# Kernel optimization log

Measured on AMD Instinct MI355X. Metric: run time of the kernel, lower is better.

Reference implementation:

```python
import jax, jax.numpy as jnp
import numpy as np

V_SIZE, E, H = 30000, 256, 128   # vocab, emb_dim, GRU hidden per direction
B, U, T, ND = 32, 32, 128, 64    # dialogues, utterances, max tokens, dialogue-id table size
SCALE = E ** 0.5                  # attention normalise_factor = hid_size**0.5, hid_size = emb_dim


def _gru_dir(x_seq, w_ih, w_hh, b_ih, b_hh):
    """Unidirectional torch-style GRU. x_seq: [N,T,E] -> [N,T,H]."""
    xp = jnp.einsum('nte,ge->ntg', x_seq, w_ih) + b_ih   # precompute input gates [N,T,3H]
    xp = jnp.swapaxes(xp, 0, 1)                          # [T,N,3H]

    def step(h, xpt):
        gh = h @ w_hh.T + b_hh
        r = jax.nn.sigmoid(xpt[:, :H] + gh[:, :H])
        z = jax.nn.sigmoid(xpt[:, H:2 * H] + gh[:, H:2 * H])
        n = jnp.tanh(xpt[:, 2 * H:] + r * gh[:, 2 * H:])
        h_new = (1.0 - z) * n + z * h
        return h_new, h_new

    h0 = jnp.zeros((x_seq.shape[0], H), x_seq.dtype)
    _, out = jax.lax.scan(step, h0, xp)
    return jnp.swapaxes(out, 0, 1)


def _forward(x, d_ids, utt_len, emb_table,
             w_ih_f, w_hh_f, b_ih_f, b_hh_f,
             w_ih_b, w_hh_b, b_ih_b, b_hh_b,
             wq, bq, wk, bk, wv, bv, wo, bo, wl, bl):
    b, u, t = x.shape
    N = b * u
    emb = emb_table[x.reshape(N, t)]                      # [N,T,E]
    lens = jnp.clip(utt_len[d_ids].reshape(N), 1, t)      # valid tokens per utterance
    pos = jnp.arange(t)
    # index map that reverses the valid prefix (padding region clipped, unused)
    rev_idx = jnp.clip(lens[:, None] - 1 - pos[None, :], 0, t - 1)  # [N,T]

    o_f = _gru_dir(emb, w_ih_f, w_hh_f, b_ih_f, b_hh_f)   # causal => correct on valid prefix
    emb_rev = jnp.take_along_axis(emb, rev_idx[:, :, None], axis=1)
    o_b = jnp.take_along_axis(_gru_dir(emb_rev, w_ih_b, w_hh_b, b_ih_b, b_hh_b),
                              rev_idx[:, :, None], axis=1)
    h = jnp.concatenate([o_f, o_b], axis=-1)              # [N,T,E] bi-GRU states

    # self-attention pooling; original takes op[-1], so only the query at the
    # last valid token (lens-1) is needed -- identical math, less compute.
    k = jnp.einsum('nte,he->nth', h, wk) + bk
    v = jnp.einsum('nte,he->nth', h, wv) + bv
    h_last = jnp.take_along_axis(h, (lens - 1)[:, None, None], axis=1)[:, 0]  # [N,E]
    q = h_last @ wq.T + bq
    score = jnp.einsum('nh,nth->nt', q, k) / SCALE
    score = jnp.where(pos[None, :] < lens[:, None], score, -jnp.inf)
    attn = jax.nn.softmax(score, axis=-1)
    ctx = jnp.einsum('nt,nth->nh', attn, v)
    out = (ctx @ wo.T + bo) @ wl.T + bl                   # make_output then final linear
    return out.reshape(b, u, -1)


def setup_inputs() -> dict:
    key = jax.random.key(0)
    ks = jax.random.split(key, 16)

    def p(k, shape):
        return (jax.random.normal(k, shape, jnp.float32) / np.sqrt(shape[-1])).astype(jnp.float32)

    return {
        'x': jax.random.randint(ks[0], (B, U, T), 0, V_SIZE, dtype=jnp.int32),
        'd_ids': jax.random.randint(ks[1], (B,), 0, ND, dtype=jnp.int32),
        'utt_len': jax.random.randint(ks[2], (ND, U), 1, T + 1, dtype=jnp.int32),
        'emb_table': p(ks[3], (V_SIZE, E)),
        'w_ih_f': p(ks[4], (3 * H, E)), 'w_hh_f': p(ks[5], (3 * H, H)),
        'b_ih_f': jnp.zeros(3 * H, jnp.float32), 'b_hh_f': jnp.zeros(3 * H, jnp.float32),
        'w_ih_b': p(ks[6], (3 * H, E)), 'w_hh_b': p(ks[7], (3 * H, H)),
        'b_ih_b': jnp.zeros(3 * H, jnp.float32), 'b_hh_b': jnp.zeros(3 * H, jnp.float32),
        'wq': p(ks[8], (E, E)), 'bq': jnp.zeros(E, jnp.float32),
        'wk': p(ks[9], (E, E)), 'bk': jnp.zeros(E, jnp.float32),
        'wv': p(ks[10], (E, E)), 'bv': jnp.zeros(E, jnp.float32),
        'wo': p(ks[11], (E, E)), 'bo': jnp.zeros(E, jnp.float32),
        'wl': p(ks[12], (E, E)), 'bl': jnp.zeros(E, jnp.float32),
    }


def reference(x, d_ids, utt_len, emb_table,
              w_ih_f, w_hh_f, b_ih_f, b_hh_f,
              w_ih_b, w_hh_b, b_ih_b, b_hh_b,
              wq, bq, wk, bk, wv, bv, wo, bo, wl, bl):
    return _forward(x, d_ids, utt_len, emb_table,
                    w_ih_f, w_hh_f, b_ih_f, b_hh_f,
                    w_ih_b, w_hh_b, b_ih_b, b_hh_b,
                    wq, bq, wk, bk, wv, bv, wo, bo, wl, bl)
```

## Files before the change

### kernel.cpp

```cpp
#include <hip/hip_runtime.h>
#include <hip/hip_bf16.h>
#include <math.h>
#include <stdint.h>

typedef unsigned short u16;
typedef unsigned int   u32;
typedef __attribute__((ext_vector_type(8))) short bf16x8;
typedef __attribute__((ext_vector_type(4))) float f32x4;

#define EDIM 256
#define HDIM 128
#define TLEN 128
#define NUTT 1024
#define UU   32
#define NBU  8

#define WS_FLAG 0
#define WS_LENS 64
#define WS_TAB  4608
#define WS_COPY 8192
#define WS_OF   18874368LL
#define WS_OB   52428800LL

#define MFMA16(a, b, c) __builtin_amdgcn_mfma_f32_16x16x32_bf16((a), (b), (c), 0, 0, 0)
#define SOUT(u, s, j) ((u) * 1096 + (s) * 136 + (j))

__constant__ int G_SZ[18] = {7680000, 98304, 49152, 384, 384, 98304, 49152, 384, 384,
                             65536, 256, 65536, 65536, 256, 65536, 256, 65536, 256};

__device__ __forceinline__ float b2f(u16 b) {
    u32 u = ((u32)b) << 16; float f; __builtin_memcpy(&f, &u, 4); return f;
}
__device__ __forceinline__ u16 f2b(float f) {
    u32 u; __builtin_memcpy(&u, &f, 4);
    u32 r = u + 0x7FFFu + ((u >> 16) & 1u);
    return (u16)(r >> 16);
}
__device__ __forceinline__ u16 f2b_hw(float f) {
    __hip_bfloat16 h = __float2bfloat16(f);
    u16 v; __builtin_memcpy(&v, &h, 2); return v;
}
__device__ __forceinline__ float fsigmoid(float x) { return 1.0f / (1.0f + __expf(-x)); }
__device__ __forceinline__ float ftanh(float x) { return 1.0f - 2.0f / (__expf(2.0f * x) + 1.0f); }

__global__ __launch_bounds__(256)
void k_convert(void* ws,
               const int* __restrict__ d_ids, const int* __restrict__ utt_len,
               const void* a0, const void* a1, const void* a2, const void* a3,
               const void* a4, const void* a5, const void* a6, const void* a7,
               const void* a8, const void* a9, const void* a10, const void* a11,
               const void* a12, const void* a13, const void* a14, const void* a15,
               const void* a16, const void* a17) {
    __shared__ int scnt[4];
    const int tid = threadIdx.x, lane = tid & 63, wid = tid >> 6;
    const u16* p = (const u16*)a0;
    int cnt = 0;
#pragma unroll 8
    for (int i = tid; i < 16384; i += 256)
        cnt += ((p[i] & 0x7F80) == 0x7F80) ? 1 : 0;
#pragma unroll
    for (int o = 32; o > 0; o >>= 1) cnt += __shfl_down(cnt, o);
    if (lane == 0) scnt[wid] = cnt;
    __syncthreads();
    const int flag = (scnt[0] + scnt[1] + scnt[2] + scnt[3] > 0) ? 1 : 0;

    if (blockIdx.x == 0) {
        if (tid == 0) {
            const void* orig[18] = {a0,a1,a2,a3,a4,a5,a6,a7,a8,a9,a10,a11,a12,a13,a14,a15,a16,a17};
            *(int*)((char*)ws + WS_FLAG) = flag;
            const u16** tab = (const u16**)((char*)ws + WS_TAB);
            char* base = (char*)ws + WS_COPY;
            long long cum = 0;
            for (int a = 0; a < 18; ++a) {
                tab[a] = flag ? (const u16*)(base + cum * 2) : (const u16*)orig[a];
                cum += G_SZ[a];
            }
        }
        int* lens = (int*)((char*)ws + WS_LENS);
#pragma unroll 4
        for (int n = tid; n < NUTT; n += 256) {
            int b = n >> 5;
            int u = n & (UU - 1);
            int L = utt_len[d_ids[b] * UU + u];
            lens[n] = min(max(L, 1), TLEN);
        }
    }

    if (flag == 0) return;
    const void* orig[18] = {a0,a1,a2,a3,a4,a5,a6,a7,a8,a9,a10,a11,a12,a13,a14,a15,a16,a17};
    u16* base = (u16*)((char*)ws + WS_COPY);
    const int gtid = blockIdx.x * blockDim.x + tid;
    const int gs   = gridDim.x * blockDim.x;
    long long cum = 0;
    for (int a = 0; a < 18; ++a) {
        const float4* src = (const float4*)orig[a];
        uint2* dst = (uint2*)(base + cum);
        const int n4 = G_SZ[a] >> 2;
        for (int i = gtid; i < n4; i += gs) {
            float4 v = src[i];
            uint2 pk;
            pk.x = (u32)f2b(v.x) | ((u32)f2b(v.y) << 16);
            pk.y = (u32)f2b(v.z) | ((u32)f2b(v.w) << 16);
            dst[i] = pk;
        }
        cum += G_SZ[a];
    }
}

__global__ __launch_bounds__(512)
void k_scan(const int* __restrict__ x, void* ws) {
    const u16* const* tab = (const u16* const*)((char*)ws + WS_TAB);
    const int dir = blockIdx.y;
    const u16* emb  = tab[0];
    const u16* w_ih = tab[1 + dir * 4];
    const u16* w_hh = tab[2 + dir * 4];
    const u16* b_ih = tab[3 + dir * 4];
    const u16* b_hh = tab[4 + dir * 4];
    u16* outp = (u16*)((char*)ws + (dir ? WS_OB : WS_OF));
    const int* lens = (const int*)((char*)ws + WS_LENS);

    const int n0 = blockIdx.x * NBU;
    __shared__ __align__(16) u16 sh_emb[2][NBU][264];
    __shared__ __align__(16) u16 sh_hi[2][NBU * 136];
    __shared__ __align__(16) u16 sh_lo[2][NBU * 136];
    __shared__ __align__(16) u16 sh_out[2][NBU * 1096];
    __shared__ int sh_tok[NBU * 132];
    __shared__ int sh_L[NBU];

    const int tid = threadIdx.x, lane = tid & 63, wvi = tid >> 6;
    const int q4 = lane >> 4, mm = lane & 15;
    const int j = wvi * 16 + mm;
    const int u8 = mm & 7;

    for (int i = tid; i < NBU * 136; i += 512) { sh_hi[0][i] = 0; sh_lo[0][i] = 0; }
    for (int i = tid; i < NBU * TLEN; i += 512) {
        const int u = i >> 7, tt = i & 127;
        sh_tok[u * 132 + tt] = x[(n0 + u) * TLEN + tt];
    }
    if (tid < NBU) sh_L[tid] = lens[n0 + tid];

    bf16x8 wih[3][8]; bf16x8 whh[3][4];
    float bcr, bcz, bxn, bgn;
#pragma unroll
    for (int n3 = 0; n3 < 3; ++n3) {
        const int g = n3 * HDIM + j;
#pragma unroll
        for (int ks = 0; ks < 8; ++ks)
            wih[n3][ks] = *(const bf16x8*)(w_ih + g * EDIM + ks * 32 + q4 * 8);
#pragma unroll
        for (int ks = 0; ks < 4; ++ks)
            whh[n3][ks] = *(const bf16x8*)(w_hh + g * HDIM + ks * 32 + q4 * 8);
    }
    bcr = b2f(b_ih[j]) + b2f(b_hh[j]);
    bcz = b2f(b_ih[HDIM + j]) + b2f(b_hh[HDIM + j]);
    bxn = b2f(b_ih[2 * HDIM + j]);
    bgn = b2f(b_hh[2 * HDIM + j]);

    const int arr0 = (q4 & 2);
    float hprev[2] = {0.f, 0.f};
    const f32x4 zero4 = {0.f, 0.f, 0.f, 0.f};
    __syncthreads();

    int Lm = sh_L[0];
#pragma unroll
    for (int u = 1; u < NBU; ++u) Lm = max(Lm, sh_L[u]);
    const int tmax = (Lm + 7) & ~7;

    const bool pwave = (wvi < 4);
    const int pf_u = lane & 7;
    const int pf_c = wvi * 8 + (lane >> 3);
    const int pf_L = sh_L[pf_u];

    uint4 pf;
    if (pwave) {
        const int te0 = dir ? (pf_L - 1) : 0;
        const int tok0 = sh_tok[pf_u * 132 + te0];
        uint4 v0 = *(const uint4*)(emb + (size_t)tok0 * EDIM + pf_c * 8);
        *(uint4*)&sh_emb[0][pf_u][pf_c * 8] = v0;
        const int te1 = dir ? max(pf_L - 2, 0) : 1;
        const int tok1 = sh_tok[pf_u * 132 + te1];
        uint4 v1 = *(const uint4*)(emb + (size_t)tok1 * EDIM + pf_c * 8);
        *(uint4*)&sh_emb[1][pf_u][pf_c * 8] = v1;
    }
    __syncthreads();

    f32x4 accx_cur[3];
    {
        bf16x8 a = *(const bf16x8*)&sh_emb[0][u8][q4 * 8];
#pragma unroll
        for (int n3 = 0; n3 < 3; ++n3) accx_cur[n3] = MFMA16(a, wih[n3][0], zero4);
#pragma unroll
        for (int ks = 1; ks < 8; ++ks) {
            bf16x8 a2 = *(const bf16x8*)&sh_emb[0][u8][ks * 32 + q4 * 8];
#pragma unroll
            for (int n3 = 0; n3 < 3; ++n3) accx_cur[n3] = MFMA16(a2, wih[n3][ks], accx_cur[n3]);
        }
    }
    __syncthreads();

    for (int t = 0; t < tmax; ++t) {
        const int cur = t & 1, nxt = cur ^ 1;
        const int obuf = (t >> 3) & 1, slot = t & 7;
        const bool more = (t + 2 < tmax);

        if (pwave && more) {
            const int te = dir ? max(pf_L - 3 - t, 0) : (t + 2);
            const int tok = sh_tok[pf_u * 132 + te];
            pf = *(const uint4*)(emb + (size_t)tok * EDIM + pf_c * 8);
        }

        f32x4 accg[3];
        {
            bf16x8 ahi = *(const bf16x8*)(sh_hi[cur] + u8 * 136 + q4 * 8);
            bf16x8 alo = *(const bf16x8*)(sh_lo[cur] + u8 * 136 + q4 * 8);
#pragma unroll
            for (int n3 = 0; n3 < 3; ++n3) {
                accg[n3] = MFMA16(ahi, whh[n3][0], zero4);
                accg[n3] = MFMA16(alo, whh[n3][0], accg[n3]);
            }
        }
#pragma unroll
        for (int ks = 1; ks < 4; ++ks) {
            bf16x8 ahi = *(const bf16x8*)(sh_hi[cur] + u8 * 136 + ks * 32 + q4 * 8);
            bf16x8 alo = *(const bf16x8*)(sh_lo[cur] + u8 * 136 + ks * 32 + q4 * 8);
#pragma unroll
            for (int n3 = 0; n3 < 3; ++n3) {
                accg[n3] = MFMA16(ahi, whh[n3][ks], accg[n3]);
                accg[n3] = MFMA16(alo, whh[n3][ks], accg[n3]);
            }
        }

        f32x4 accx_nxt[3];
        if (t + 1 < tmax) {
            bf16x8 a = *(const bf16x8*)&sh_emb[nxt][u8][q4 * 8];
#pragma unroll
            for (int n3 = 0; n3 < 3; ++n3) accx_nxt[n3] = MFMA16(a, wih[n3][0], zero4);
#pragma unroll
            for (int ks = 1; ks < 8; ++ks) {
                bf16x8 a2 = *(const bf16x8*)&sh_emb[nxt][u8][ks * 32 + q4 * 8];
#pragma unroll
                for (int n3 = 0; n3 < 3; ++n3) accx_nxt[n3] = MFMA16(a2, wih[n3][ks], accx_nxt[n3]);
            }
        }

#pragma unroll
        for (int rr2 = 0; rr2 < 2; ++rr2) {
            const int arr = rr2 + arr0;
            const int u   = (q4 * 4 + arr) & 7;
            const float r  = fsigmoid(accx_cur[0][arr] + accg[0][arr] + bcr);
            const float z  = fsigmoid(accx_cur[1][arr] + accg[1][arr] + bcz);
            const float nn = ftanh((accx_cur[2][arr] + bxn) + r * (accg[2][arr] + bgn));
            const float hn = (1.0f - z) * nn + z * hprev[rr2];
            hprev[rr2] = hn;
            const u16 hb = f2b_hw(hn);
            sh_hi[nxt][u * 136 + j] = hb;
            sh_lo[nxt][u * 136 + j] = f2b_hw(hn - b2f(hb));
            sh_out[obuf][SOUT(u, slot, j)] = hb;
        }

        if (pwave && more)
            *(uint4*)&sh_emb[cur][pf_u][pf_c * 8] = pf;

        if (t + 1 < tmax) {
#pragma unroll
            for (int n3 = 0; n3 < 3; ++n3) accx_cur[n3] = accx_nxt[n3];
        }

        __syncthreads();

        if (slot == 7) {
            const int rowIdx = tid >> 3;
            const int part   = tid & 7;
            const int fu = rowIdx >> 3, fs = rowIdx & 7;
            const int tt = (t & ~7) + fs;
            const int tout = dir ? (sh_L[fu] - 1 - tt) : tt;
            if (tout >= 0) {
                const u16* srcp = &sh_out[obuf][SOUT(fu, fs, part * 16)];
                uint4 v0 = *(const uint4*)(srcp);
                uint4 v1 = *(const uint4*)(srcp + 8);
                u16* dstp = outp + ((size_t)(n0 + fu) * TLEN + tout) * HDIM + part * 16;
                *(uint4*)(dstp)     = v0;
                *(uint4*)(dstp + 8) = v1;
            }
        }
    }
}

__global__ __launch_bounds__(256)
void k_attn(void* ws, void* outv) {
    const u16* const* tab = (const u16* const*)((char*)ws + WS_TAB);
    const u16* wq = tab[9];  const u16* bq = tab[10];
    const u16* wk = tab[11];
    const u16* wv = tab[12]; const u16* bv = tab[13];
    const u16* wo = tab[14]; const u16* bo = tab[15];
    const u16* wl = tab[16]; const u16* bl = tab[17];
    const int* lens = (const int*)((char*)ws + WS_LENS);
    const int flag = *(const int*)((const char*)ws + WS_FLAG);

    const int n = blockIdx.x;
    const int L = lens[n];
    const u16* hf = (const u16*)((char*)ws + WS_OF) + (size_t)n * TLEN * HDIM;
    const u16* hb = (const u16*)((char*)ws + WS_OB) + (size_t)n * TLEN * HDIM;

    __shared__ float sh_hl[EDIM];
    __shared__ float sh_v1[EDIM];
    __shared__ float sh_uv[EDIM];
    __shared__ float sh_a[4 * EDIM];
    __shared__ float sh_m[4], sh_l[4];

    const int tid = threadIdx.x, lane = tid & 63, wid = tid >> 6;

    sh_hl[tid] = (tid < HDIM) ? b2f(hf[(size_t)(L - 1) * HDIM + tid])
                              : b2f(hb[(size_t)(L - 1) * HDIM + (tid - HDIM)]);
    __syncthreads();

    {
        float s0 = b2f(bq[tid]), s1 = 0.0f;
        const u16* wr = wq + tid * EDIM;
#pragma unroll
        for (int ks = 0; ks < 32; ks += 2) {
            bf16x8 w8 = *(const bf16x8*)(wr + ks * 8);
            bf16x8 w9 = *(const bf16x8*)(wr + ks * 8 + 8);
#pragma unroll
            for (int d = 0; d < 8; ++d) {
                s0 += b2f((u16)w8[d]) * sh_hl[ks * 8 + d];
                s1 += b2f((u16)w9[d]) * sh_hl[ks * 8 + 8 + d];
            }
        }
        sh_v1[tid] = s0 + s1;
    }
    __syncthreads();

    {
        float s0 = 0.0f, s1 = 0.0f;
        for (int i = 0; i < EDIM; i += 2) {
            s0 += b2f(wk[i * EDIM + tid]) * sh_v1[i];
            s1 += b2f(wk[(i + 1) * EDIM + tid]) * sh_v1[i + 1];
        }
        sh_uv[tid] = s0 + s1;
    }
    __syncthreads();

    {
        const int e0 = lane * 4;
        const float u0 = sh_uv[e0], u1 = sh_uv[e0 + 1];
        const float u2 = sh_uv[e0 + 2], u3 = sh_uv[e0 + 3];
        float m = -1e30f, l = 0.0f;
        float a0 = 0.f, a1 = 0.f, a2 = 0.f, a3 = 0.f;
        for (int t = wid; t < L; t += 4) {
            const u16* src = (lane < 32) ? (hf + (size_t)t * HDIM + lane * 4)
                                         : (hb + (size_t)t * HDIM + (lane - 32) * 4);
            uint2 pv = *(const uint2*)src;
            const float h0 = b2f((u16)(pv.x & 0xFFFF));
            const float h1 = b2f((u16)(pv.x >> 16));
            const float h2 = b2f((u16)(pv.y & 0xFFFF));
            const float h3 = b2f((u16)(pv.y >> 16));
            float p = h0 * u0 + h1 * u1 + h2 * u2 + h3 * u3;
#pragma unroll
            for (int o = 32; o > 0; o >>= 1) p += __shfl_xor(p, o);
            const float s = p * 0.0625f;
            const float mn = fmaxf(m, s);
            const float c = __expf(m - mn);
            const float w = __expf(s - mn);
            l = l * c + w;
            a0 = a0 * c + w * h0;
            a1 = a1 * c + w * h1;
            a2 = a2 * c + w * h2;
            a3 = a3 * c + w * h3;
            m = mn;
        }
        sh_a[wid * EDIM + e0]     = a0;
        sh_a[wid * EDIM + e0 + 1] = a1;
        sh_a[wid * EDIM + e0 + 2] = a2;
        sh_a[wid * EDIM + e0 + 3] = a3;
        if (lane == 0) { sh_m[wid] = m; sh_l[wid] = l; }
    }
    __syncthreads();

    {
        const float m0 = sh_m[0], m1 = sh_m[1], m2 = sh_m[2], m3 = sh_m[3];
        const float M = fmaxf(fmaxf(m0, m1), fmaxf(m2, m3));
        const float c0 = __expf(m0 - M), c1 = __expf(m1 - M);
        const float c2 = __expf(m2 - M), c3 = __expf(m3 - M);
        const float den = c0 * sh_l[0] + c1 * sh_l[1] + c2 * sh_l[2] + c3 * sh_l[3];
        const float num = c0 * sh_a[tid] + c1 * sh_a[EDIM + tid] +
                          c2 * sh_a[2 * EDIM + tid] + c3 * sh_a[3 * EDIM + tid];
        sh_hl[tid] = num / den;
    }
    __syncthreads();

    {
        float s0 = b2f(bv[tid]), s1 = 0.0f;
        const u16* wr = wv + tid * EDIM;
#pragma unroll
        for (int ks = 0; ks < 32; ks += 2) {
            bf16x8 w8 = *(const bf16x8*)(wr + ks * 8);
            bf16x8 w9 = *(const bf16x8*)(wr + ks * 8 + 8);
#pragma unroll
            for (int d = 0; d < 8; ++d) {
                s0 += b2f((u16)w8[d]) * sh_hl[ks * 8 + d];
                s1 += b2f((u16)w9[d]) * sh_hl[ks * 8 + 8 + d];
            }
        }
        sh_uv[tid] = s0 + s1;
    }
    __syncthreads();

    {
        float s0 = b2f(bo[tid]), s1 = 0.0f;
        const u16* wr = wo + tid * EDIM;
#pragma unroll
        for (int ks = 0; ks < 32; ks += 2) {
            bf16x8 w8 = *(const bf16x8*)(wr + ks * 8);
            bf16x8 w9 = *(const bf16x8*)(wr + ks * 8 + 8);
#pragma unroll
            for (int d = 0; d < 8; ++d) {
                s0 += b2f((u16)w8[d]) * sh_uv[ks * 8 + d];
                s1 += b2f((u16)w9[d]) * sh_uv[ks * 8 + 8 + d];
            }
        }
        sh_v1[tid] = s0 + s1;
    }
    __syncthreads();

    {
        float s0 = b2f(bl[tid]), s1 = 0.0f;
        const u16* wr = wl + tid * EDIM;
#pragma unroll
        for (int ks = 0; ks < 32; ks += 2) {
            bf16x8 w8 = *(const bf16x8*)(wr + ks * 8);
            bf16x8 w9 = *(const bf16x8*)(wr + ks * 8 + 8);
#pragma unroll
            for (int d = 0; d < 8; ++d) {
                s0 += b2f((u16)w8[d]) * sh_v1[ks * 8 + d];
                s1 += b2f((u16)w9[d]) * sh_v1[ks * 8 + 8 + d];
            }
        }
        const float s = s0 + s1;
        const size_t oidx = (size_t)n * EDIM + tid;
        if (flag) ((float*)outv)[oidx] = s;
        else      ((u16*)outv)[oidx]   = f2b(s);
    }
}

extern "C" void kernel_launch(void* const* d_in, const int* in_sizes, int n_in,
                              void* d_out, int out_size, void* d_ws, size_t ws_size,
                              hipStream_t stream) {
    const int* x       = (const int*)d_in[0];
    const int* d_ids   = (const int*)d_in[1];
    const int* utt_len = (const int*)d_in[2];
    const void* f_arr[18] = {
        d_in[3],
        d_in[4], d_in[5], d_in[6], d_in[7],
        d_in[8], d_in[9], d_in[10], d_in[11],
        d_in[12], d_in[13],
        d_in[14],
        d_in[16], d_in[17],
        d_in[18], d_in[19],
        d_in[20], d_in[21]
    };

    k_convert<<<512, 256, 0, stream>>>(d_ws, d_ids, utt_len,
        f_arr[0], f_arr[1], f_arr[2], f_arr[3], f_arr[4], f_arr[5], f_arr[6], f_arr[7],
        f_arr[8], f_arr[9], f_arr[10], f_arr[11], f_arr[12], f_arr[13], f_arr[14],
        f_arr[15], f_arr[16], f_arr[17]);

    k_scan<<<dim3(NUTT / NBU, 2), 512, 0, stream>>>(x, d_ws);

    k_attn<<<NUTT, 256, 0, stream>>>(d_ws, d_out);
}
```

Measured before the change: 410.3 us.

## Pack hi/lo and two timesteps into unused MFMA rows of GRU recurrence

The GRU recurrence kernel previously used only 8 of the 16 MFMA rows, so each step issued separate hi and lo matmuls for the hidden state and a separate input projection. It now puts the hi and lo halves in rows 0-7 and 8-15 of one MFMA and sums them with a cross-lane shuffle, halving the recurrent MFMA count. The input projection for two timesteps is computed in one MFMA and split by shuffles. The loop is unrolled by two with a single prefetch stage, and all 8 waves now take part in the embedding prefetch. The cost is extra shuffles and select logic, and the prefetch is exposed less often, which may add latency.

Result: faster. 370.5 us (-9.7%).

```diff
diff --git a/kernel.cpp b/kernel.cpp
--- a/kernel.cpp
+++ b/kernel.cpp
@@ -131,6 +131,9 @@
     const int q4 = lane >> 4, mm = lane & 15;
     const int j = wvi * 16 + mm;
     const int u8 = mm & 7;
+    const int arr0 = (q4 & 2);
+    const bool a2 = (arr0 != 0);
+    const bool lo32 = (lane < 32);
 
     for (int i = tid; i < NBU * 136; i += 512) { sh_hi[0][i] = 0; sh_lo[0][i] = 0; }
     for (int i = tid; i < NBU * TLEN; i += 512) {
@@ -156,7 +159,6 @@
     bxn = b2f(b_ih[2 * HDIM + j]);
     bgn = b2f(b_hh[2 * HDIM + j]);
 
-    const int arr0 = (q4 & 2);
     float hprev[2] = {0.f, 0.f};
     const f32x4 zero4 = {0.f, 0.f, 0.f, 0.f};
     __syncthreads();
@@ -166,113 +168,146 @@
     for (int u = 1; u < NBU; ++u) Lm = max(Lm, sh_L[u]);
     const int tmax = (Lm + 7) & ~7;
 
-    const bool pwave = (wvi < 4);
     const int pf_u = lane & 7;
-    const int pf_c = wvi * 8 + (lane >> 3);
+    const int pf_c = (wvi & 3) * 8 + (lane >> 3);
     const int pf_L = sh_L[pf_u];
-
-    uint4 pf;
-    if (pwave) {
-        const int te0 = dir ? (pf_L - 1) : 0;
-        const int tok0 = sh_tok[pf_u * 132 + te0];
-        uint4 v0 = *(const uint4*)(emb + (size_t)tok0 * EDIM + pf_c * 8);
-        *(uint4*)&sh_emb[0][pf_u][pf_c * 8] = v0;
-        const int te1 = dir ? max(pf_L - 2, 0) : 1;
-        const int tok1 = sh_tok[pf_u * 132 + te1];
-        uint4 v1 = *(const uint4*)(emb + (size_t)tok1 * EDIM + pf_c * 8);
-        *(uint4*)&sh_emb[1][pf_u][pf_c * 8] = v1;
-    }
-    __syncthreads();
-
-    f32x4 accx_cur[3];
-    {
-        bf16x8 a = *(const bf16x8*)&sh_emb[0][u8][q4 * 8];
-#pragma unroll
-        for (int n3 = 0; n3 < 3; ++n3) accx_cur[n3] = MFMA16(a, wih[n3][0], zero4);
-#pragma unroll
-        for (int ks = 1; ks < 8; ++ks) {
-            bf16x8 a2 = *(const bf16x8*)&sh_emb[0][u8][ks * 32 + q4 * 8];
-#pragma unroll
-            for (int n3 = 0; n3 < 3; ++n3) accx_cur[n3] = MFMA16(a2, wih[n3][ks], accx_cur[n3]);
-        }
-    }
-    __syncthreads();
-
-    for (int t = 0; t < tmax; ++t) {
-        const int cur = t & 1, nxt = cur ^ 1;
-        const int obuf = (t >> 3) & 1, slot = t & 7;
-        const bool more = (t + 2 < tmax);
-
-        if (pwave && more) {
-            const int te = dir ? max(pf_L - 3 - t, 0) : (t + 2);
+    const int tsel = wvi >> 2;
+
+    {
+        const int te = dir ? max(pf_L - 1 - tsel, 0) : tsel;
+        const int tok = sh_tok[pf_u * 132 + te];
+        uint4 v = *(const uint4*)(emb + (size_t)tok * EDIM + pf_c * 8);
+        *(uint4*)&sh_emb[tsel][pf_u][pf_c * 8] = v;
+    }
+    __syncthreads();
+
+    for (int t0 = 0; t0 < tmax; t0 += 2) {
+        const int obuf = (t0 >> 3) & 1;
+        const bool more = (t0 + 2 < tmax);
+
+        uint4 pf;
+        if (more) {
+            const int tt = t0 + 2 + tsel;
+            const int te = dir ? max(pf_L - 1 - tt, 0) : tt;
             const int tok = sh_tok[pf_u * 132 + te];
             pf = *(const uint4*)(emb + (size_t)tok * EDIM + pf_c * 8);
         }
 
-        f32x4 accg[3];
+        f32x4 accx[3];
         {
-            bf16x8 ahi = *(const bf16x8*)(sh_hi[cur] + u8 * 136 + q4 * 8);
-            bf16x8 alo = *(const bf16x8*)(sh_lo[cur] + u8 * 136 + q4 * 8);
-#pragma unroll
-            for (int n3 = 0; n3 < 3; ++n3) {
-                accg[n3] = MFMA16(ahi, whh[n3][0], zero4);
-                accg[n3] = MFMA16(alo, whh[n3][0], accg[n3]);
-            }
-        }
-#pragma unroll
-        for (int ks = 1; ks < 4; ++ks) {
-            bf16x8 ahi = *(const bf16x8*)(sh_hi[cur] + u8 * 136 + ks * 32 + q4 * 8);
-            bf16x8 alo = *(const bf16x8*)(sh_lo[cur] + u8 * 136 + ks * 32 + q4 * 8);
-#pragma unroll
-            for (int n3 = 0; n3 < 3; ++n3) {
-                accg[n3] = MFMA16(ahi, whh[n3][ks], accg[n3]);
-                accg[n3] = MFMA16(alo, whh[n3][ks], accg[n3]);
-            }
-        }
-
-        f32x4 accx_nxt[3];
-        if (t + 1 < tmax) {
-            bf16x8 a = *(const bf16x8*)&sh_emb[nxt][u8][q4 * 8];
-#pragma unroll
-            for (int n3 = 0; n3 < 3; ++n3) accx_nxt[n3] = MFMA16(a, wih[n3][0], zero4);
+            const u16* eb_ = (mm < 8) ? &sh_emb[0][u8][0] : &sh_emb[1][u8][0];
+            bf16x8 a = *(const bf16x8*)(eb_ + q4 * 8);
+            accx[0] = MFMA16(a, wih[0][0], zero4);
+            accx[1] = MFMA16(a, wih[1][0], zero4);
+            accx[2] = MFMA16(a, wih[2][0], zero4);
 #pragma unroll
             for (int ks = 1; ks < 8; ++ks) {
-                bf16x8 a2 = *(const bf16x8*)&sh_emb[nxt][u8][ks * 32 + q4 * 8];
-#pragma unroll
-                for (int n3 = 0; n3 < 3; ++n3) accx_nxt[n3] = MFMA16(a2, wih[n3][ks], accx_nxt[n3]);
-            }
-        }
-
-#pragma unroll
-        for (int rr2 = 0; rr2 < 2; ++rr2) {
-            const int arr = rr2 + arr0;
-            const int u   = (q4 * 4 + arr) & 7;
-            const float r  = fsigmoid(accx_cur[0][arr] + accg[0][arr] + bcr);
-            const float z  = fsigmoid(accx_cur[1][arr] + accg[1][arr] + bcz);
-            const float nn = ftanh((accx_cur[2][arr] + bxn) + r * (accg[2][arr] + bgn));
-            const float hn = (1.0f - z) * nn + z * hprev[rr2];
-            hprev[rr2] = hn;
-            const u16 hb = f2b_hw(hn);
-            sh_hi[nxt][u * 136 + j] = hb;
-            sh_lo[nxt][u * 136 + j] = f2b_hw(hn - b2f(hb));
-            sh_out[obuf][SOUT(u, slot, j)] = hb;
-        }
-
-        if (pwave && more)
-            *(uint4*)&sh_emb[cur][pf_u][pf_c * 8] = pf;
-
-        if (t + 1 < tmax) {
-#pragma unroll
-            for (int n3 = 0; n3 < 3; ++n3) accx_cur[n3] = accx_nxt[n3];
-        }
-
+                bf16x8 av = *(const bf16x8*)(eb_ + ks * 32 + q4 * 8);
+                accx[0] = MFMA16(av, wih[0][ks], accx[0]);
+                accx[1] = MFMA16(av, wih[1][ks], accx[1]);
+                accx[2] = MFMA16(av, wih[2][ks], accx[2]);
+            }
+        }
+        float xA[3][2], xB[3][2];
+#pragma unroll
+        for (int g = 0; g < 3; ++g) {
+#pragma unroll
+            for (int r = 0; r < 2; ++r) {
+                const float sv = a2 ? accx[g][r] : accx[g][2 + r];
+                const float ov = a2 ? accx[g][2 + r] : accx[g][r];
+                const float pv = __shfl_xor(sv, 32);
+                xA[g][r] = lo32 ? ov : pv;
+                xB[g][r] = lo32 ? pv : ov;
+            }
+        }
+
+        {
+            f32x4 accg[3];
+            const u16* hb_ = ((mm < 8) ? sh_hi[0] : sh_lo[0]) + u8 * 136;
+            {
+                bf16x8 a = *(const bf16x8*)(hb_ + q4 * 8);
+                accg[0] = MFMA16(a, whh[0][0], zero4);
+                accg[1] = MFMA16(a, whh[1][0], zero4);
+                accg[2] = MFMA16(a, whh[2][0], zero4);
+            }
+#pragma unroll
+            for (int ks = 1; ks < 4; ++ks) {
+                bf16x8 a = *(const bf16x8*)(hb_ + ks * 32 + q4 * 8);
+                accg[0] = MFMA16(a, whh[0][ks], accg[0]);
+                accg[1] = MFMA16(a, whh[1][ks], accg[1]);
+                accg[2] = MFMA16(a, whh[2][ks], accg[2]);
+            }
+            const int slot = t0 & 7;
+#pragma unroll
+            for (int r = 0; r < 2; ++r) {
+                float gg[3];
+#pragma unroll
+                for (int g = 0; g < 3; ++g) {
+                    const float sv = a2 ? accg[g][r] : accg[g][2 + r];
+                    const float ov = a2 ? accg[g][2 + r] : accg[g][r];
+                    gg[g] = ov + __shfl_xor(sv, 32);
+                }
+                const int u = (q4 * 4 + arr0 + r) & 7;
+                const float rg = fsigmoid(xA[0][r] + gg[0] + bcr);
+                const float zg = fsigmoid(xA[1][r] + gg[1] + bcz);
+                const float nn = ftanh((xA[2][r] + bxn) + rg * (gg[2] + bgn));
+                const float hn = (1.0f - zg) * nn + zg * hprev[r];
+                hprev[r] = hn;
+                const u16 hb16 = f2b_hw(hn);
+                sh_hi[1][u * 136 + j] = hb16;
+                sh_lo[1][u * 136 + j] = f2b_hw(hn - b2f(hb16));
+                sh_out[obuf][SOUT(u, slot, j)] = hb16;
+            }
+        }
         __syncthreads();
 
-        if (slot == 7) {
+        {
+            f32x4 accg[3];
+            const u16* hb_ = ((mm < 8) ? sh_hi[1] : sh_lo[1]) + u8 * 136;
+            {
+                bf16x8 a = *(const bf16x8*)(hb_ + q4 * 8);
+                accg[0] = MFMA16(a, whh[0][0], zero4);
+                accg[1] = MFMA16(a, whh[1][0], zero4);
+                accg[2] = MFMA16(a, whh[2][0], zero4);
+            }
+#pragma unroll
+            for (int ks = 1; ks < 4; ++ks) {
+                bf16x8 a = *(const bf16x8*)(hb_ + ks * 32 + q4 * 8);
+                accg[0] = MFMA16(a, whh[0][ks], accg[0]);
+                accg[1] = MFMA16(a, whh[1][ks], accg[1]);
+                accg[2] = MFMA16(a, whh[2][ks], accg[2]);
+            }
+            const int slot = (t0 & 7) + 1;
+#pragma unroll
+            for (int r = 0; r < 2; ++r) {
+                float gg[3];
+#pragma unroll
+                for (int g = 0; g < 3; ++g) {
+                    const float sv = a2 ? accg[g][r] : accg[g][2 + r];
+                    const float ov = a2 ? accg[g][2 + r] : accg[g][r];
+                    gg[g] = ov + __shfl_xor(sv, 32);
+                }
+                const int u = (q4 * 4 + arr0 + r) & 7;
+                const float rg = fsigmoid(xB[0][r] + gg[0] + bcr);
+                const float zg = fsigmoid(xB[1][r] + gg[1] + bcz);
+                const float nn = ftanh((xB[2][r] + bxn) + rg * (gg[2] + bgn));
+                const float hn = (1.0f - zg) * nn + zg * hprev[r];
+                hprev[r] = hn;
+                const u16 hb16 = f2b_hw(hn);
+                sh_hi[0][u * 136 + j] = hb16;
+                sh_lo[0][u * 136 + j] = f2b_hw(hn - b2f(hb16));
+                sh_out[obuf][SOUT(u, slot, j)] = hb16;
+            }
+        }
+        if (more)
+            *(uint4*)&sh_emb[tsel][pf_u][pf_c * 8] = pf;
+        __syncthreads();
+
+        if (((t0 + 1) & 7) == 7) {
             const int rowIdx = tid >> 3;
             const int part   = tid & 7;
             const int fu = rowIdx >> 3, fs = rowIdx & 7;
-            const int tt = (t & ~7) + fs;
+            const int tt = ((t0 + 1) & ~7) + fs;
             const int tout = dir ? (sh_L[fu] - 1 - tt) : tt;
             if (tout >= 0) {
                 const u16* srcp = &sh_out[obuf][SOUT(fu, fs, part * 16)];
```
